# Kernel tuning notes

Measured on AMD Instinct MI355X. Metric: run time of the kernel, lower is better.

Reference implementation:

```python
import jax, jax.numpy as jnp
import numpy as np

B, S, D, H, L = 16, 1024, 128, 8, 3
DFF = 4 * D  # 512
DH = D // H  # 16
NUM_CLASSES = 6


def layernorm(x, g, b, eps):
    mu = jnp.mean(x, axis=-1, keepdims=True)
    var = jnp.mean(jnp.square(x - mu), axis=-1, keepdims=True)
    return g * (x - mu) / jnp.sqrt(var + eps) + b


def setup_inputs() -> dict:
    key = jax.random.key(0)
    ks = jax.random.split(key, 16)
    sc = 0.05
    inp = {
        'x': jax.random.normal(ks[0], (B, S, D), dtype=jnp.float32),
        'Wq': jax.random.normal(ks[1], (L, D, D), dtype=jnp.float32) * sc,
        'bq': jnp.zeros((L, D), dtype=jnp.float32),
        'Wk': jax.random.normal(ks[2], (L, D, D), dtype=jnp.float32) * sc,
        'bk': jnp.zeros((L, D), dtype=jnp.float32),
        'Wv': jax.random.normal(ks[3], (L, D, D), dtype=jnp.float32) * sc,
        'bv': jnp.zeros((L, D), dtype=jnp.float32),
        'ln1_g': jnp.ones((L, D), dtype=jnp.float32),
        'ln1_b': jnp.zeros((L, D), dtype=jnp.float32),
        'W1': jax.random.normal(ks[4], (L, D, DFF), dtype=jnp.float32) * sc,
        'b1': jnp.zeros((L, DFF), dtype=jnp.float32),
        'W2': jax.random.normal(ks[5], (L, DFF, D), dtype=jnp.float32) * sc,
        'b2': jnp.zeros((L, D), dtype=jnp.float32),
        'ln2_g': jnp.ones((L, D), dtype=jnp.float32),
        'ln2_b': jnp.zeros((L, D), dtype=jnp.float32),
        'Wout': jax.random.normal(ks[6], (D, NUM_CLASSES), dtype=jnp.float32) * sc,
        'bout': jnp.zeros((NUM_CLASSES,), dtype=jnp.float32),
    }
    return inp


def reference(x, Wq, bq, Wk, bk, Wv, bv, ln1_g, ln1_b, W1, b1, W2, b2, ln2_g, ln2_b, Wout, bout):
    scale = 1.0 / jnp.sqrt(jnp.float32(DH))
    for l in range(L):
        # Q/K/V projections with ReLU activation (as in source Dense(..., relu))
        q = jax.nn.relu(jnp.einsum('bsd,de->bse', x, Wq[l]) + bq[l])
        k = jax.nn.relu(jnp.einsum('bsd,de->bse', x, Wk[l]) + bk[l])
        v = jax.nn.relu(jnp.einsum('bsd,de->bse', x, Wv[l]) + bv[l])
        # split-heads (tf.split axis=-1 / concat axis=0 == reshape to heads)
        qh = q.reshape(B, S, H, DH)
        kh = k.reshape(B, S, H, DH)
        vh = v.reshape(B, S, H, DH)
        scores = jnp.einsum('bqhd,bkhd->bhqk', qh, kh) * scale  # [B,H,S,S]
        attn = jax.nn.softmax(scores, axis=-1)
        o = jnp.einsum('bhqk,bkhd->bqhd', attn, vh).reshape(B, S, D)
        x = layernorm(o + x, ln1_g[l], ln1_b[l], 1e-8)
        # pointwise FFN (Conv1D kernel_size=1 == dense over last dim)
        h = jax.nn.relu(jnp.einsum('bsd,df->bsf', x, W1[l]) + b1[l])
        f = jnp.einsum('bsf,fd->bsd', h, W2[l]) + b2[l]
        x = layernorm(f + x, ln2_g[l], ln2_b[l], 1e-6)
    return jnp.einsum('bsd,dc->bsc', x, Wout) + bout
```

## Files before the change

kernel.cpp:

```cpp
#include <hip/hip_runtime.h>
#include <math.h>

#define Bq 16
#define Sq 1024
#define Dq 128
#define Hq 8
#define DHq 16
#define DFFq 512
#define Lq 3
#define NCLS 6
#define NROWS (Bq * Sq)
#define NX ((size_t)NROWS * Dq)

#define QSCL 0.36067376022224085f

typedef __attribute__((ext_vector_type(8))) short    bf16x8;
typedef __attribute__((ext_vector_type(4))) float    f32x4;
typedef __attribute__((ext_vector_type(4))) _Float16 f16x4;
typedef __attribute__((ext_vector_type(8))) _Float16 f16x8;
typedef __attribute__((ext_vector_type(2))) _Float16 f16x2;

__device__ inline ushort f32_to_bf16(float f) {
    union { float f; unsigned u; } v; v.f = f;
    unsigned r = v.u + 0x7fffu + ((v.u >> 16) & 1u);
    return (ushort)(r >> 16);
}

__device__ __forceinline__ float exp2_raw(float x) {
    float r;
    asm("v_exp_f32 %0, %1" : "=v"(r) : "v"(x));
    return r;
}

__device__ __forceinline__ float rcp_fast(float x) {
    float r;
    asm("v_rcp_f32 %0, %1" : "=v"(r) : "v"(x));
    return r;
}

__device__ __forceinline__ f16x2 pkrtz(float a, float b) {
    return __builtin_bit_cast(f16x2, __builtin_amdgcn_cvt_pkrtz(a, b));
}

__global__ __launch_bounds__(256) void prep_kernel(
    const float* __restrict__ Wqp, const float* __restrict__ Wkp,
    const float* __restrict__ Wvp, const float* __restrict__ W1p,
    const float* __restrict__ W2p, const float* __restrict__ xp,
    ushort* __restrict__ wbf, ushort* __restrict__ xbf)
{
    const int gid = blockIdx.x * 256 + threadIdx.x;
    if (gid < 147456) {
        const int w   = gid / 49152;
        const int rem = gid - w * 49152;
        const int l   = rem >> 14;
        const int idx = rem & 16383;
        const int k   = idx >> 7;
        const int n   = idx & 127;
        const float* src = (w == 0) ? Wqp : (w == 1) ? Wkp : Wvp;
        const float scl = (w == 0) ? QSCL : 1.0f;
        wbf[(size_t)(w * 3 + l) * 16384 + n * 128 + k] =
            f32_to_bf16(src[(size_t)l * 16384 + k * 128 + n] * scl);
    } else if (gid < 344064) {
        const int g   = gid - 147456;
        const int l   = g >> 16;
        const int idx = g & 65535;
        const int k   = idx >> 9;
        const int n   = idx & 511;
        wbf[147456 + (size_t)l * 65536 + n * 128 + k] =
            f32_to_bf16(W1p[(size_t)l * 65536 + k * 512 + n]);
    } else if (gid < 540672) {
        const int g   = gid - 344064;
        const int l   = g >> 16;
        const int idx = g & 65535;
        const int k   = idx >> 7;
        const int n   = idx & 127;
        wbf[344064 + (size_t)l * 65536 + n * 512 + k] =
            f32_to_bf16(W2p[(size_t)l * 65536 + k * 128 + n]);
    } else {
        const int g = gid - 540672;
        xbf[g] = f32_to_bf16(xp[g]);
    }
}

__global__ __launch_bounds__(256) void gemm_qkv(
    const ushort* __restrict__ A,
    const ushort* __restrict__ wq, const ushort* __restrict__ wk,
    const ushort* __restrict__ wv,
    const float* __restrict__ bqp, const float* __restrict__ bkp,
    const float* __restrict__ bvp,
    _Float16* __restrict__ qo, _Float16* __restrict__ ko,
    _Float16* __restrict__ vo)
{
    __shared__ ushort As[64 * 40];
    __shared__ ushort Bs[128 * 40];

    const int sel  = blockIdx.y;
    const ushort* Bt   = (sel == 0) ? wq : (sel == 1) ? wk : wv;
    const float*  bias = (sel == 0) ? bqp : (sel == 1) ? bkp : bvp;
    const float   bscl = (sel == 0) ? QSCL : 1.0f;

    const int tid  = threadIdx.x;
    const int row0 = blockIdx.x * 64;
    const int wave = tid >> 6;
    const int lane = tid & 63;
    const int quad = lane >> 4;
    const int m16  = lane & 15;
    const int wm   = wave >> 1;
    const int wn   = wave & 1;

    const int sar = tid >> 2;
    const int sac = (tid & 3) * 8;

    f32x4 acc[2][4];
    #pragma unroll
    for (int i = 0; i < 2; ++i)
        #pragma unroll
        for (int j = 0; j < 4; ++j) acc[i][j] = (f32x4)0.f;

    const int r1 = tid >> 2, r2 = r1 + 64;

    bf16x8 av  = *(const bf16x8*)(A  + (size_t)(row0 + sar) * 128 + sac);
    bf16x8 bv1 = *(const bf16x8*)(Bt + (size_t)r1 * 128 + sac);
    bf16x8 bv2 = *(const bf16x8*)(Bt + (size_t)r2 * 128 + sac);

    for (int k0 = 0; k0 < 128; k0 += 32) {
        __syncthreads();
        *(bf16x8*)&As[sar * 40 + sac] = av;
        *(bf16x8*)&Bs[r1 * 40 + sac]  = bv1;
        *(bf16x8*)&Bs[r2 * 40 + sac]  = bv2;
        __syncthreads();

        if (k0 < 96) {
            av  = *(const bf16x8*)(A  + (size_t)(row0 + sar) * 128 + k0 + 32 + sac);
            bv1 = *(const bf16x8*)(Bt + (size_t)r1 * 128 + k0 + 32 + sac);
            bv2 = *(const bf16x8*)(Bt + (size_t)r2 * 128 + k0 + 32 + sac);
        }

        bf16x8 af[2], bf[4];
        #pragma unroll
        for (int i = 0; i < 2; ++i)
            af[i] = *(const bf16x8*)&As[(32 * wm + 16 * i + m16) * 40 + quad * 8];
        #pragma unroll
        for (int j = 0; j < 4; ++j)
            bf[j] = *(const bf16x8*)&Bs[(64 * wn + 16 * j + m16) * 40 + quad * 8];
        #pragma unroll
        for (int i = 0; i < 2; ++i)
            #pragma unroll
            for (int j = 0; j < 4; ++j)
                acc[i][j] = __builtin_amdgcn_mfma_f32_16x16x32_bf16(af[i], bf[j], acc[i][j], 0, 0, 0);
    }

    #pragma unroll
    for (int i = 0; i < 2; ++i) {
        #pragma unroll
        for (int j = 0; j < 4; ++j) {
            const int col = 64 * wn + 16 * j + m16;
            const float bb = bias[col] * bscl;
            const int hh = col >> 4, dh = col & 15;
            #pragma unroll
            for (int r = 0; r < 4; ++r) {
                float val = fmaxf(acc[i][j][r] + bb, 0.f);
                const int gr = row0 + 32 * wm + 16 * i + quad * 4 + r;
                const int b = gr >> 10, s = gr & 1023;
                if (sel == 2) {
                    vo[(((size_t)b * Hq + hh) * DHq + dh) * Sq + s] = (_Float16)val;
                } else {
                    _Float16* outp = (sel == 0) ? qo : ko;
                    outp[(((size_t)b * Hq + hh) * Sq + s) * DHq + dh] = (_Float16)val;
                }
            }
        }
    }
}

__global__ __launch_bounds__(256, 3) void gemm_ffn_fused(
    const _Float16* __restrict__ o, const float* __restrict__ resid,
    const float* __restrict__ g1, const float* __restrict__ beta1,
    const ushort* __restrict__ W1t, const float* __restrict__ bias1,
    const ushort* __restrict__ W2t, const float* __restrict__ bias2,
    const float* __restrict__ g2, const float* __restrict__ beta2,
    float* __restrict__ xb,
    const ushort* __restrict__ wqn, const ushort* __restrict__ wkn,
    const ushort* __restrict__ wvn,
    const float* __restrict__ bqn, const float* __restrict__ bkn,
    const float* __restrict__ bvn,
    _Float16* __restrict__ qo, _Float16* __restrict__ ko,
    _Float16* __restrict__ vo, int do_next,
    const float* __restrict__ Wout, const float* __restrict__ bout,
    float* __restrict__ out, int last)
{
    __shared__ __align__(16) char smem[44544];
    ushort*    Af   = (ushort*)smem;
    ushort*    Hcc  = (ushort*)(smem + 8704);
    ushort*    Bs   = (ushort*)(smem + 17408);
    float*     wo_s = (float*)(smem + 17408);
    _Float16*  vals = (_Float16*)(smem + 35840);
    float*     mus  = (float*)(smem + 44288);
    float*     rsds = (float*)(smem + 44416);

    const int tid  = threadIdx.x;
    const int row0 = blockIdx.x * 32;
    const int wave = tid >> 6;
    const int lane = tid & 63;
    const int quad = lane >> 4;
    const int m16  = lane & 15;
    const int wm   = wave >> 1;
    const int wn   = wave & 1;
    const int sac  = (tid & 3) * 8;
    const int r1   = tid >> 2, r2 = r1 + 64;

    const int ca = lane * 2;
    const float2 gg  = *(const float2*)(g1 + ca);
    const float2 bt1 = *(const float2*)(beta1 + ca);
    f16x2  ovv[8];
    float2 rvv[8];
    #pragma unroll
    for (int it = 0; it < 8; ++it) {
        const size_t base = (size_t)(row0 + wave * 8 + it) * Dq;
        ovv[it] = *(const f16x2*)(o + base + ca);
        rvv[it] = *(const float2*)(resid + base + ca);
    }
    #pragma unroll
    for (int it = 0; it < 8; ++it) {
        const int rr = wave * 8 + it;
        const float v0 = (float)ovv[it][0] + rvv[it].x;
        const float v1 = (float)ovv[it][1] + rvv[it].y;

        float s = v0 + v1;
        #pragma unroll
        for (int off = 32; off > 0; off >>= 1) s += __shfl_xor(s, off, 64);
        const float mu = s * (1.f / 128.f);
        const float d0 = v0 - mu, d1 = v1 - mu;
        float vs = d0 * d0 + d1 * d1;
        #pragma unroll
        for (int off = 32; off > 0; off >>= 1) vs += __shfl_xor(vs, off, 64);
        const float rstd = rsqrtf(vs * (1.f / 128.f) + 1e-8f);

        const float rv0 = gg.x * d0 * rstd + bt1.x;
        const float rv1 = gg.y * d1 * rstd + bt1.y;
        ushort2 ab; ab.x = f32_to_bf16(rv0); ab.y = f32_to_bf16(rv1);
        *(ushort2*)&Af[rr * 136 + ca] = ab;
        f16x2 vv; vv[0] = (_Float16)rv0; vv[1] = (_Float16)rv1;
        *(f16x2*)&vals[rr * 132 + ca] = vv;
    }

    f32x4 acc[4], acc2[4];
    #pragma unroll
    for (int j = 0; j < 4; ++j) { acc[j] = (f32x4)0.f; acc2[j] = (f32x4)0.f; }

    bf16x8 w11 = *(const bf16x8*)(W1t + (size_t)r1 * 128 + sac);
    bf16x8 w12 = *(const bf16x8*)(W1t + (size_t)r1 * 128 + 32 + sac);
    bf16x8 w21 = *(const bf16x8*)(W1t + (size_t)r2 * 128 + sac);
    bf16x8 w22 = *(const bf16x8*)(W1t + (size_t)r2 * 128 + 32 + sac);

    #pragma unroll
    for (int t = 0; t < 16; ++t) {
        const int cc   = t >> 2;
        const int ph   = (t >> 1) & 1;
        const int half = t & 1;

        __syncthreads();
        *(bf16x8*)&Bs[r1 * 72 + sac]      = w11;
        *(bf16x8*)&Bs[r1 * 72 + 32 + sac] = w12;
        *(bf16x8*)&Bs[r2 * 72 + sac]      = w21;
        *(bf16x8*)&Bs[r2 * 72 + 32 + sac] = w22;
        __syncthreads();

        if (t < 15) {
            const int tn  = t + 1;
            const int nc  = tn >> 2, np = (tn >> 1) & 1, nh = tn & 1;
            if (np == 0) {
                const ushort* p = W1t + (size_t)(nc * 128) * 128 + nh * 64;
                w11 = *(const bf16x8*)(p + (size_t)r1 * 128 + sac);
                w12 = *(const bf16x8*)(p + (size_t)r1 * 128 + 32 + sac);
                w21 = *(const bf16x8*)(p + (size_t)r2 * 128 + sac);
                w22 = *(const bf16x8*)(p + (size_t)r2 * 128 + 32 + sac);
            } else {
                const ushort* p = W2t + nc * 128 + nh * 64;
                w11 = *(const bf16x8*)(p + (size_t)r1 * 512 + sac);
                w12 = *(const bf16x8*)(p + (size_t)r1 * 512 + 32 + sac);
                w21 = *(const bf16x8*)(p + (size_t)r2 * 512 + sac);
                w22 = *(const bf16x8*)(p + (size_t)r2 * 512 + 32 + sac);
            }
        } else if (do_next) {
            w11 = *(const bf16x8*)(wqn + (size_t)r1 * 128 + sac);
            w12 = *(const bf16x8*)(wqn + (size_t)r1 * 128 + 32 + sac);
            w21 = *(const bf16x8*)(wqn + (size_t)r2 * 128 + sac);
            w22 = *(const bf16x8*)(wqn + (size_t)r2 * 128 + 32 + sac);
        }

        const ushort* Asrc = ph ? Hcc : Af;
        #pragma unroll
        for (int hh = 0; hh < 2; ++hh) {
            const int kk = half * 64 + hh * 32;
            const bf16x8 af = *(const bf16x8*)&Asrc[(16 * wm + m16) * 136 + kk + quad * 8];
            bf16x8 bf[4];
            #pragma unroll
            for (int j = 0; j < 4; ++j)
                bf[j] = *(const bf16x8*)&Bs[(64 * wn + 16 * j + m16) * 72 + hh * 32 + quad * 8];
            if (ph == 0) {
                #pragma unroll
                for (int j = 0; j < 4; ++j)
                    acc[j] = __builtin_amdgcn_mfma_f32_16x16x32_bf16(af, bf[j], acc[j], 0, 0, 0);
            } else {
                #pragma unroll
                for (int j = 0; j < 4; ++j)
                    acc2[j] = __builtin_amdgcn_mfma_f32_16x16x32_bf16(af, bf[j], acc2[j], 0, 0, 0);
            }
        }

        if (ph == 0 && half == 1) {
            #pragma unroll
            for (int j = 0; j < 4; ++j) {
                const int col_l = 64 * wn + 16 * j + m16;
                const float bb = bias1[cc * 128 + col_l];
                #pragma unroll
                for (int r = 0; r < 4; ++r) {
                    const int row = 16 * wm + quad * 4 + r;
                    Hcc[row * 136 + col_l] = f32_to_bf16(fmaxf(acc[j][r] + bb, 0.f));
                }
                acc[j] = (f32x4)0.f;
            }
        }
    }

    __syncthreads();

    float vreg[4][4];
    #pragma unroll
    for (int j = 0; j < 4; ++j) {
        const int col = 64 * wn + 16 * j + m16;
        const float bb = bias2[col];
        #pragma unroll
        for (int r = 0; r < 4; ++r) {
            const int row = 16 * wm + quad * 4 + r;
            float v = acc2[j][r] + bb + (float)vals[row * 132 + col];
            vreg[j][r] = v;
            vals[row * 132 + col] = (_Float16)v;
        }
    }
    if (last) {
        #pragma unroll
        for (int i = 0; i < 3; ++i) wo_s[tid + i * 256] = Wout[tid + i * 256];
    }
    __syncthreads();

    {
        const int row = tid >> 3;
        const int c0  = (tid & 7) * 16;
        float s = 0.f, s2 = 0.f;
        #pragma unroll
        for (int u = 0; u < 4; ++u) {
            const f16x4 xv = *(const f16x4*)&vals[row * 132 + c0 + u * 4];
            #pragma unroll
            for (int e = 0; e < 4; ++e) {
                const float x = (float)xv[e];
                s += x; s2 = fmaf(x, x, s2);
            }
        }
        s  += __shfl_xor(s, 1, 64);  s  += __shfl_xor(s, 2, 64);  s  += __shfl_xor(s, 4, 64);
        s2 += __shfl_xor(s2, 1, 64); s2 += __shfl_xor(s2, 2, 64); s2 += __shfl_xor(s2, 4, 64);
        if ((tid & 7) == 0) {
            const float mu  = s * (1.f / 128.f);
            const float var = s2 * (1.f / 128.f) - mu * mu;
            mus[row]  = mu;
            rsds[row] = rsqrtf(var + 1e-6f);
        }
    }
    __syncthreads();

    if (!last) {
        #pragma unroll
        for (int j = 0; j < 4; ++j) {
            const int col = 64 * wn + 16 * j + m16;
            #pragma unroll
            for (int r = 0; r < 4; ++r) {
                const int row = 16 * wm + quad * 4 + r;
                const float rn = g2[col] * (vreg[j][r] - mus[row]) * rsds[row] + beta2[col];
                xb[(size_t)(row0 + row) * Dq + col] = rn;
                Af[row * 136 + col] = f32_to_bf16(rn);
            }
        }

        if (do_next) {
            f32x4 qacc[4];
            #pragma unroll
            for (int st = 0; st < 6; ++st) {
                const int sel  = st >> 1;
                const int half = st & 1;
                if (half == 0) {
                    #pragma unroll
                    for (int j = 0; j < 4; ++j) qacc[j] = (f32x4)0.f;
                }

                __syncthreads();
                *(bf16x8*)&Bs[r1 * 72 + sac]      = w11;
                *(bf16x8*)&Bs[r1 * 72 + 32 + sac] = w12;
                *(bf16x8*)&Bs[r2 * 72 + sac]      = w21;
                *(bf16x8*)&Bs[r2 * 72 + 32 + sac] = w22;
                __syncthreads();

                if (st < 5) {
                    const int sel2 = (st + 1) >> 1;
                    const int k02  = ((st + 1) & 1) * 64;
                    const ushort* Bt2 = (sel2 == 0) ? wqn : (sel2 == 1) ? wkn : wvn;
                    w11 = *(const bf16x8*)(Bt2 + (size_t)r1 * 128 + k02 + sac);
                    w12 = *(const bf16x8*)(Bt2 + (size_t)r1 * 128 + k02 + 32 + sac);
                    w21 = *(const bf16x8*)(Bt2 + (size_t)r2 * 128 + k02 + sac);
                    w22 = *(const bf16x8*)(Bt2 + (size_t)r2 * 128 + k02 + 32 + sac);
                }

                const int k0 = half * 64;
                #pragma unroll
                for (int hh = 0; hh < 2; ++hh) {
                    const int kk = k0 + hh * 32;
                    const bf16x8 af = *(const bf16x8*)&Af[(16 * wm + m16) * 136 + kk + quad * 8];
                    bf16x8 bf[4];
                    #pragma unroll
                    for (int j = 0; j < 4; ++j)
                        bf[j] = *(const bf16x8*)&Bs[(64 * wn + 16 * j + m16) * 72 + hh * 32 + quad * 8];
                    #pragma unroll
                    for (int j = 0; j < 4; ++j)
                        qacc[j] = __builtin_amdgcn_mfma_f32_16x16x32_bf16(af, bf[j], qacc[j], 0, 0, 0);
                }

                if (half) {
                    const float* bias = (sel == 0) ? bqn : (sel == 1) ? bkn : bvn;
                    const float  bscl = (sel == 0) ? QSCL : 1.0f;
                    #pragma unroll
                    for (int j = 0; j < 4; ++j) {
                        const int col = 64 * wn + 16 * j + m16;
                        const float bb = bias[col] * bscl;
                        const int hh = col >> 4, dh = col & 15;
                        #pragma unroll
                        for (int r = 0; r < 4; ++r) {
                            float val = fmaxf(qacc[j][r] + bb, 0.f);
                            const int gr = row0 + 16 * wm + quad * 4 + r;
                            const int b = gr >> 10, s = gr & 1023;
                            if (sel == 2) {
                                vo[(((size_t)b * Hq + hh) * DHq + dh) * Sq + s] = (_Float16)val;
                            } else {
                                _Float16* outp = (sel == 0) ? qo : ko;
                                outp[(((size_t)b * Hq + hh) * Sq + s) * DHq + dh] = (_Float16)val;
                            }
                        }
                    }
                }
            }
        }
    } else {
        #pragma unroll
        for (int j = 0; j < 4; ++j) {
            const int col = 64 * wn + 16 * j + m16;
            #pragma unroll
            for (int r = 0; r < 4; ++r) {
                const int row = 16 * wm + quad * 4 + r;
                vals[row * 132 + col] =
                    (_Float16)(g2[col] * (vreg[j][r] - mus[row]) * rsds[row] + beta2[col]);
            }
        }
        __syncthreads();
        if (tid < 32 * NCLS) {
            const int row = tid / NCLS;
            const int c   = tid - row * NCLS;
            float a = bout[c];
            #pragma unroll 8
            for (int kk = 0; kk < Dq; ++kk)
                a = fmaf((float)vals[row * 132 + kk], wo_s[kk * NCLS + c], a);
            out[(size_t)(row0 + row) * NCLS + c] = a;
        }
    }
}

__global__ __launch_bounds__(256) void attn_mfma(
    const _Float16* __restrict__ q, const _Float16* __restrict__ k,
    const _Float16* __restrict__ vt, _Float16* __restrict__ o)
{
    __shared__ _Float16 Ks[256 * 20];
    __shared__ _Float16 Vs[16 * 264];

    const int bh   = blockIdx.x;
    const int qc   = blockIdx.y;
    const int b    = bh >> 3;
    const int h    = bh & 7;
    const int tid  = threadIdx.x;
    const int wave = tid >> 6;
    const int lane = tid & 63;
    const int quad = lane >> 4;
    const int m16  = lane & 15;
    const int q0   = qc * 64 + wave * 16;

    const f16x4 qf0 = *(const f16x4*)(q + (((size_t)bh * Sq) + q0 + m16) * DHq + quad * 4);

    const _Float16* kg  = k  + (size_t)bh * Sq * DHq;
    const _Float16* vtg = vt + (size_t)bh * DHq * Sq;

    f32x4 oacc0 = (f32x4)0.f;
    f32x4 dacc0 = (f32x4)0.f;

    f16x4 onesf;
    onesf[0] = (_Float16)1.f; onesf[1] = (_Float16)1.f;
    onesf[2] = (_Float16)1.f; onesf[3] = (_Float16)1.f;

    const int krow = tid;
    const int vrow = tid >> 4;
    const int vcol = (tid & 15) * 16;

    f16x8 ka  = *(const f16x8*)(kg + (size_t)krow * DHq);
    f16x8 kb8 = *(const f16x8*)(kg + (size_t)krow * DHq + 8);
    f16x8 va  = *(const f16x8*)(vtg + (size_t)vrow * Sq + vcol);
    f16x8 vb  = *(const f16x8*)(vtg + (size_t)vrow * Sq + vcol + 8);

    for (int kb = 0; kb < 4; ++kb) {
        __syncthreads();
        *(f16x8*)&Ks[krow * 20 + 0] = ka;
        *(f16x8*)&Ks[krow * 20 + 8] = kb8;
        *(f16x8*)&Vs[vrow * 264 + vcol + 0] = va;
        *(f16x8*)&Vs[vrow * 264 + vcol + 8] = vb;
        __syncthreads();

        if (kb < 3) {
            const _Float16* kp = kg  + ((size_t)(kb + 1) * 256 + krow) * DHq;
            const _Float16* vp = vtg + (size_t)vrow * Sq + (kb + 1) * 256 + vcol;
            ka  = *(const f16x8*)(kp);
            kb8 = *(const f16x8*)(kp + 8);
            va  = *(const f16x8*)(vp);
            vb  = *(const f16x8*)(vp + 8);
        }

        __builtin_amdgcn_s_setprio(1);
        #pragma unroll 4
        for (int kt = 0; kt < 16; ++kt) {
            const f16x4 kf = *(const f16x4*)&Ks[(kt * 16 + m16) * 20 + quad * 4];
            const f16x4 vf = *(const f16x4*)&Vs[m16 * 264 + kt * 16 + quad * 4];

            f32x4 st0 = __builtin_amdgcn_mfma_f32_16x16x16f16(kf, qf0, (f32x4)0.f, 0, 0, 0);

            const f16x2 a0 = pkrtz(exp2_raw(st0[0]), exp2_raw(st0[1]));
            const f16x2 a1 = pkrtz(exp2_raw(st0[2]), exp2_raw(st0[3]));
            const f16x4 pf0 = __builtin_shufflevector(a0, a1, 0, 1, 2, 3);

            oacc0 = __builtin_amdgcn_mfma_f32_16x16x16f16(pf0, vf, oacc0, 0, 0, 0);
            dacc0 = __builtin_amdgcn_mfma_f32_16x16x16f16(pf0, onesf, dacc0, 0, 0, 0);
        }
        __builtin_amdgcn_s_setprio(0);
    }

    #pragma unroll
    for (int r = 0; r < 4; ++r) {
        const float i0 = rcp_fast(dacc0[r]);
        o[((size_t)b * Sq + q0 + quad * 4 + r) * Dq + h * DHq + m16] = (_Float16)(oacc0[r] * i0);
    }
}

extern "C" void kernel_launch(void* const* d_in, const int* in_sizes, int n_in,
                              void* d_out, int out_size, void* d_ws, size_t ws_size,
                              hipStream_t stream)
{
    const float* x_in  = (const float*)d_in[0];
    const float* Wq    = (const float*)d_in[1];
    const float* bq    = (const float*)d_in[2];
    const float* Wk    = (const float*)d_in[3];
    const float* bk    = (const float*)d_in[4];
    const float* Wv    = (const float*)d_in[5];
    const float* bv    = (const float*)d_in[6];
    const float* ln1_g = (const float*)d_in[7];
    const float* ln1_b = (const float*)d_in[8];
    const float* W1    = (const float*)d_in[9];
    const float* b1    = (const float*)d_in[10];
    const float* W2    = (const float*)d_in[11];
    const float* b2    = (const float*)d_in[12];
    const float* ln2_g = (const float*)d_in[13];
    const float* ln2_b = (const float*)d_in[14];
    const float* Wout  = (const float*)d_in[15];
    const float* bout  = (const float*)d_in[16];
    float* out = (float*)d_out;

    float* ws = (float*)d_ws;
    _Float16* qf16 = (_Float16*)ws;
    _Float16* kf16 = (_Float16*)(ws + NX / 2);
    _Float16* vt16 = (_Float16*)(ws + NX);
    float*    xb   = ws + 9 * NX / 2;
    ushort*   xbf0 = (ushort*)(ws + 11 * NX / 2);
    ushort*   wbf  = (ushort*)(ws + 7 * NX);
    _Float16* obuf = (_Float16*)(ws + 8 * NX);

    prep_kernel<<<dim3(10304), dim3(256), 0, stream>>>(Wq, Wk, Wv, W1, W2, x_in, wbf, xbf0);

    const dim3 blk(256);

    {
        const ushort* wqt = wbf + (size_t)0 * 16384;
        const ushort* wkt = wbf + (size_t)3 * 16384;
        const ushort* wvt = wbf + (size_t)6 * 16384;
        gemm_qkv<<<dim3(256, 3), blk, 0, stream>>>(
            xbf0, wqt, wkt, wvt, bq, bk, bv, qf16, kf16, vt16);
    }

    const float* xcur = x_in;
    for (int l = 0; l < Lq; ++l) {
        const ushort* w1t = wbf + 147456 + (size_t)l * 65536;
        const ushort* w2t = wbf + 344064 + (size_t)l * 65536;
        const int next = (l < Lq - 1) ? 1 : 0;
        const int ln   = l + 1;
        const ushort* wqn = next ? (wbf + (size_t)(0 * 3 + ln) * 16384) : wbf;
        const ushort* wkn = next ? (wbf + (size_t)(1 * 3 + ln) * 16384) : wbf;
        const ushort* wvn = next ? (wbf + (size_t)(2 * 3 + ln) * 16384) : wbf;
        const float*  bqn = next ? (bq + ln * Dq) : bq;
        const float*  bkn = next ? (bk + ln * Dq) : bk;
        const float*  bvn = next ? (bv + ln * Dq) : bv;

        attn_mfma<<<dim3(Bq * Hq, 16), blk, 0, stream>>>(qf16, kf16, vt16, obuf);

        gemm_ffn_fused<<<dim3(512), blk, 0, stream>>>(
            obuf, xcur, ln1_g + l * Dq, ln1_b + l * Dq,
            w1t, b1 + l * DFFq, w2t, b2 + l * Dq,
            ln2_g + l * Dq, ln2_b + l * Dq,
            xb,
            wqn, wkn, wvn, bqn, bkn, bvn,
            qf16, kf16, vt16, next,
            Wout, bout, out, (l == Lq - 1) ? 1 : 0);

        xcur = xb;
    }
}
```

Before: 246.4 us.

## Process four query tiles per wave in attention to reuse K/V tiles

Each wave now computes four 16-row query tiles instead of one, so each block covers 256 queries and the grid shrinks fourfold. Each K/V tile staged in shared memory is reused across more queries, which reduces global and LDS load traffic per query. Issuing four independent MFMA chains also helps hide latency. The trade-off is higher register pressure, fewer blocks to fill the GPU, and a smaller unroll of the inner loop.

Result: no change. 249.7 us (+1.3%).

```diff
diff --git a/kernel.cpp b/kernel.cpp
--- a/kernel.cpp
+++ b/kernel.cpp
@@ -488,15 +488,19 @@
     const int lane = tid & 63;
     const int quad = lane >> 4;
     const int m16  = lane & 15;
-    const int q0   = qc * 64 + wave * 16;
-
-    const f16x4 qf0 = *(const f16x4*)(q + (((size_t)bh * Sq) + q0 + m16) * DHq + quad * 4);
+    const int q0   = qc * 256 + wave * 64;
+
+    f16x4 qf[4];
+    #pragma unroll
+    for (int i = 0; i < 4; ++i)
+        qf[i] = *(const f16x4*)(q + (((size_t)bh * Sq) + q0 + i * 16 + m16) * DHq + quad * 4);
 
     const _Float16* kg  = k  + (size_t)bh * Sq * DHq;
     const _Float16* vtg = vt + (size_t)bh * DHq * Sq;
 
-    f32x4 oacc0 = (f32x4)0.f;
-    f32x4 dacc0 = (f32x4)0.f;
+    f32x4 oacc[4], dacc[4];
+    #pragma unroll
+    for (int i = 0; i < 4; ++i) { oacc[i] = (f32x4)0.f; dacc[i] = (f32x4)0.f; }
 
     f16x4 onesf;
     onesf[0] = (_Float16)1.f; onesf[1] = (_Float16)1.f;
@@ -529,27 +533,36 @@
         }
 
         __builtin_amdgcn_s_setprio(1);
-        #pragma unroll 4
+        #pragma unroll 2
         for (int kt = 0; kt < 16; ++kt) {
             const f16x4 kf = *(const f16x4*)&Ks[(kt * 16 + m16) * 20 + quad * 4];
             const f16x4 vf = *(const f16x4*)&Vs[m16 * 264 + kt * 16 + quad * 4];
 
-            f32x4 st0 = __builtin_amdgcn_mfma_f32_16x16x16f16(kf, qf0, (f32x4)0.f, 0, 0, 0);
-
-            const f16x2 a0 = pkrtz(exp2_raw(st0[0]), exp2_raw(st0[1]));
-            const f16x2 a1 = pkrtz(exp2_raw(st0[2]), exp2_raw(st0[3]));
-            const f16x4 pf0 = __builtin_shufflevector(a0, a1, 0, 1, 2, 3);
-
-            oacc0 = __builtin_amdgcn_mfma_f32_16x16x16f16(pf0, vf, oacc0, 0, 0, 0);
-            dacc0 = __builtin_amdgcn_mfma_f32_16x16x16f16(pf0, onesf, dacc0, 0, 0, 0);
+            f32x4 st[4];
+            #pragma unroll
+            for (int i = 0; i < 4; ++i)
+                st[i] = __builtin_amdgcn_mfma_f32_16x16x16f16(kf, qf[i], (f32x4)0.f, 0, 0, 0);
+
+            #pragma unroll
+            for (int i = 0; i < 4; ++i) {
+                const f16x2 a0 = pkrtz(exp2_raw(st[i][0]), exp2_raw(st[i][1]));
+                const f16x2 a1 = pkrtz(exp2_raw(st[i][2]), exp2_raw(st[i][3]));
+                const f16x4 pf = __builtin_shufflevector(a0, a1, 0, 1, 2, 3);
+                oacc[i] = __builtin_amdgcn_mfma_f32_16x16x16f16(pf, vf, oacc[i], 0, 0, 0);
+                dacc[i] = __builtin_amdgcn_mfma_f32_16x16x16f16(pf, onesf, dacc[i], 0, 0, 0);
+            }
         }
         __builtin_amdgcn_s_setprio(0);
     }
 
     #pragma unroll
-    for (int r = 0; r < 4; ++r) {
-        const float i0 = rcp_fast(dacc0[r]);
-        o[((size_t)b * Sq + q0 + quad * 4 + r) * Dq + h * DHq + m16] = (_Float16)(oacc0[r] * i0);
+    for (int i = 0; i < 4; ++i) {
+        #pragma unroll
+        for (int r = 0; r < 4; ++r) {
+            const float inv = rcp_fast(dacc[i][r]);
+            o[((size_t)b * Sq + q0 + i * 16 + quad * 4 + r) * Dq + h * DHq + m16] =
+                (_Float16)(oacc[i][r] * inv);
+        }
     }
 }
 
@@ -610,7 +623,7 @@
         const float*  bkn = next ? (bk + ln * Dq) : bk;
         const float*  bvn = next ? (bv + ln * Dq) : bv;
 
-        attn_mfma<<<dim3(Bq * Hq, 16), blk, 0, stream>>>(qf16, kf16, vt16, obuf);
+        attn_mfma<<<dim3(Bq * Hq, 4), blk, 0, stream>>>(qf16, kf16, vt16, obuf);
 
         gemm_ffn_fused<<<dim3(512), blk, 0, stream>>>(
             obuf, xcur, ln1_g + l * Dq, ln1_b + l * Dq,
```
